# Kernel tuning notes

Measured on AMD Instinct MI355X. Metric: run time of the kernel, lower is better.

The kernel has to match this reference:

```python
import jax, jax.numpy as jnp
import numpy as np

D_MODEL = 1024
H = 16
D_K = D_MODEL // H
NEG = -1.0e9


def setup_inputs() -> dict:
    key = jax.random.key(0)
    ks = jax.random.split(key, 12)
    B, S = 2, 2048
    s = 1.0 / np.sqrt(D_MODEL)
    inp = {
        "q": jax.random.normal(ks[0], (B, S, D_MODEL), jnp.float32),
        "k": jax.random.normal(ks[1], (B, S, D_MODEL), jnp.float32),
        "v": jax.random.normal(ks[2], (B, S, D_MODEL), jnp.float32),
        "mask": jnp.tril(jnp.ones((S, S), jnp.int32))[None, None, :, :],
        "wq": jax.random.normal(ks[3], (D_MODEL, D_MODEL), jnp.float32) * s,
        "bq": jax.random.normal(ks[4], (D_MODEL,), jnp.float32) * s,
        "wk": jax.random.normal(ks[5], (D_MODEL, D_MODEL), jnp.float32) * s,
        "bk": jax.random.normal(ks[6], (D_MODEL,), jnp.float32) * s,
        "wv": jax.random.normal(ks[7], (D_MODEL, D_MODEL), jnp.float32) * s,
        "bv": jax.random.normal(ks[8], (D_MODEL,), jnp.float32) * s,
        "wo": jax.random.normal(ks[9], (D_MODEL, D_MODEL), jnp.float32) * s,
        "bo": jax.random.normal(ks[10], (D_MODEL,), jnp.float32) * s,
    }
    return inp


def _split_heads(x):
    # [B,S,D] -> [B,H,S,d_k]
    B, S, _ = x.shape
    return x.reshape(B, S, H, D_K).transpose(0, 2, 1, 3)


def reference(q, k, v, mask, wq, bq, wk, bk, wv, bv, wo, bo):
    # torch Linear: y = x @ W.T + b
    query = _split_heads(q @ wq.T + bq)
    key = _split_heads(k @ wk.T + bk)
    value = _split_heads(v @ wv.T + bv)
    # scores: [B,H,S,S]
    scores = jnp.einsum("bhqd,bhkd->bhqk", query, key) / jnp.sqrt(
        jnp.asarray(D_K, query.dtype))
    scores = jnp.where(mask == 0, jnp.asarray(NEG, scores.dtype), scores)
    attn = jax.nn.softmax(scores, axis=-1)  # dropout p=0.0 -> identity
    x = jnp.einsum("bhqk,bhkd->bhqd", attn, value)
    B, _, S, _ = x.shape
    x = x.transpose(0, 2, 1, 3).reshape(B, S, D_MODEL)
    return x @ wo.T + bo
```

## Files before the change

kernel.cpp:

```cpp
#include <hip/hip_runtime.h>
#include <hip/hip_bf16.h>
#include <cstdint>
#include <cstddef>

#define BATCH 2
#define SEQ   2048
#define DM    1024
#define NH    16
#define DK    64
#define MROWS (BATCH*SEQ)

typedef __bf16 bf16;
typedef float  f32x4  __attribute__((ext_vector_type(4)));
typedef bf16   bf16x8 __attribute__((ext_vector_type(8)));
typedef bf16   bf16x4 __attribute__((ext_vector_type(4)));

#define MFMA32(a, b, c) __builtin_amdgcn_mfma_f32_16x16x32_bf16(a, b, c, 0, 0, 0)

__device__ __forceinline__ void llds16(const void* gc, void* l) {
    void* g = (void*)gc;
    __builtin_amdgcn_global_load_lds(
        (__attribute__((address_space(1))) uint32_t*)g,
        (__attribute__((address_space(3))) uint32_t*)l,
        16, 0, 0);
}

__global__ __launch_bounds__(256) void k_convert(
    const float* __restrict__ q, const float* __restrict__ k, const float* __restrict__ v,
    const float* __restrict__ wq, const float* __restrict__ wk, const float* __restrict__ wv,
    const float* __restrict__ wo,
    bf16* __restrict__ qb, bf16* __restrict__ kb, bf16* __restrict__ vb,
    bf16* __restrict__ wqb, bf16* __restrict__ wkb, bf16* __restrict__ wvb,
    bf16* __restrict__ wob) {
    long t = (long)blockIdx.x * blockDim.x + threadIdx.x;
    const long NQ = (long)MROWS * DM / 4;
    const long NW = (long)DM * DM / 4;
    const float* src; bf16* dst; long off;
    if (t < NQ)            { src = q;  dst = qb;  off = t; }
    else if (t < 2*NQ)     { src = k;  dst = kb;  off = t - NQ; }
    else if (t < 3*NQ)     { src = v;  dst = vb;  off = t - 2*NQ; }
    else {
        long u = t - 3*NQ;
        if (u < NW)        { src = wq; dst = wqb; off = u; }
        else if (u < 2*NW) { src = wk; dst = wkb; off = u - NW; }
        else if (u < 3*NW) { src = wv; dst = wvb; off = u - 2*NW; }
        else               { src = wo; dst = wob; off = u - 3*NW; }
    }
    f32x4 x = *(const f32x4*)(src + off * 4);
    bf16x4 y;
    y[0] = (bf16)x[0]; y[1] = (bf16)x[1]; y[2] = (bf16)x[2]; y[3] = (bf16)x[3];
    *(bf16x4*)(dst + off * 4) = y;
}

__global__ __launch_bounds__(512, 8) void k_gemm_qkv(
    const bf16* __restrict__ qb, const bf16* __restrict__ kb, const bf16* __restrict__ vb,
    const bf16* __restrict__ wqb, const bf16* __restrict__ wkb, const bf16* __restrict__ wvb,
    const float* __restrict__ bq, const float* __restrict__ bk, const float* __restrict__ bv,
    bf16* __restrict__ Qf, bf16* __restrict__ Kf, bf16* __restrict__ Vf) {
    const int z = blockIdx.z;
    const int bid = blockIdx.x;
    const bf16* A; const bf16* B; const float* bias;
    int m0, n0;
    if (z == 2) {
        A = vb; B = wvb; bias = bv;
        m0 = (bid >> 4) * 128;
        n0 = (bid & 15) * 64;
    } else {
        A = z ? wkb : wqb; B = z ? kb : qb; bias = z ? bk : bq;
        m0 = (bid >> 6) * 128;
        n0 = (bid & 63) * 64;
    }

    constexpr int K = DM, BK = 64;
    __shared__ bf16 sA[128 * BK];
    __shared__ bf16 sB[64 * BK];
    const int tid = threadIdx.x;
    const int l = tid & 63, w = tid >> 6;
    const int quad = l >> 4, l15 = l & 15;
    const int wm = w & 1, wn = w >> 1;
    const int srow = l >> 3;
    const int scol = ((l & 7) ^ srow) * 8;

    f32x4 acc[4] = {};
    for (int k0 = 0; k0 < K; k0 += BK) {
#pragma unroll
        for (int i = 0; i < 2; ++i) {
            int g8 = (w * 2 + i) * 8;
            llds16(A + (size_t)(m0 + g8 + srow) * K + k0 + scol, &sA[g8 * BK]);
        }
        {
            int g8 = w * 8;
            llds16(B + (size_t)(n0 + g8 + srow) * K + k0 + scol, &sB[g8 * BK]);
        }
        __syncthreads();

#pragma unroll
        for (int kk = 0; kk < 2; ++kk) {
            bf16x8 af[4], bfr;
            {
                int row = wn * 16 + l15;
                int byt = (row * 128 + kk * 64 + quad * 16) ^ ((row & 7) << 4);
                bfr = *(const bf16x8*)((const char*)sB + byt);
            }
#pragma unroll
            for (int mi = 0; mi < 4; ++mi) {
                int row = wm * 64 + mi * 16 + l15;
                int byt = (row * 128 + kk * 64 + quad * 16) ^ ((row & 7) << 4);
                af[mi] = *(const bf16x8*)((const char*)sA + byt);
            }
#pragma unroll
            for (int mi = 0; mi < 4; ++mi)
                acc[mi] = MFMA32(af[mi], bfr, acc[mi]);
        }
        __syncthreads();
    }

    if (z == 2) {
        int dcol = n0 + wn * 16 + l15;
        int hh2 = dcol >> 6;
        int dtile = (dcol >> 4) & 3;
        float bias_v = bias[dcol];
#pragma unroll
        for (int mi = 0; mi < 4; ++mi) {
            int srw = m0 + wm * 64 + mi * 16;
            int bb = srw >> 11, sl = srw & 2047;
            int kc = sl >> 5;
            bf16x4 pack;
#pragma unroll
            for (int r = 0; r < 4; ++r)
                pack[r] = (bf16)(acc[mi][r] + bias_v);
            size_t entry = ((size_t)(bb * NH + hh2) * 64 + kc) * 4 + dtile;
            *(bf16x4*)(Vf + entry * 512 + (size_t)(quad * 16 + l15) * 8 + (mi & 1) * 4) = pack;
        }
    } else {
        bf16* out = z ? Kf : Qf;
        const float scale = z ? 1.0f : 0.18033688f;
        int scolg = n0 + wn * 16 + l15;
        int bb = scolg >> 11, s = scolg & 2047;
        int s16 = s >> 4;
#pragma unroll
        for (int mi = 0; mi < 4; ++mi) {
            int drow = m0 + wm * 64 + mi * 16;
            int hh2 = (drow >> 6) & 15;
            int chunk = (drow & 63) >> 5;
            int qp = 2 * (mi & 1) + (quad >> 1);
            bf16x4 pack;
#pragma unroll
            for (int r = 0; r < 4; ++r)
                pack[r] = (bf16)((acc[mi][r] + bias[drow + quad * 4 + r]) * scale);
            size_t entry = ((size_t)(bb * NH + hh2) * 128 + s16) * 2 + chunk;
            *(bf16x4*)(out + entry * 512 + (size_t)(qp * 16 + l15) * 8 + (quad & 1) * 4) = pack;
        }
    }
}

__global__ __launch_bounds__(512, 4) void k_gemm_out(
    const bf16* __restrict__ X, const bf16* __restrict__ wob,
    const float* __restrict__ bo, float* __restrict__ out) {
    constexpr int K = DM, BK = 64, NS = K / BK;
    const int m0 = blockIdx.y * 128, n0 = blockIdx.x * 64;
    __shared__ bf16 sA[2][128 * BK];
    __shared__ bf16 sB[2][64 * BK];
    const int tid = threadIdx.x;
    const int l = tid & 63, w = tid >> 6;
    const int quad = l >> 4, l15 = l & 15;
    const int wm = w & 1, wn = w >> 1;
    const int srow = l >> 3;
    const int scol = ((l & 7) ^ srow) * 8;

#pragma unroll
    for (int i = 0; i < 2; ++i) {
        int g8 = (w * 2 + i) * 8;
        llds16(X + (size_t)(m0 + g8 + srow) * K + scol, &sA[0][g8 * BK]);
    }
    llds16(wob + (size_t)(n0 + w * 8 + srow) * K + scol, &sB[0][(w * 8) * BK]);

    f32x4 acc[4] = {};
    for (int s = 0; s < NS; ++s) {
        __syncthreads();
        const int cur = s & 1;
        if (s + 1 < NS) {
            const int k0 = (s + 1) * BK;
#pragma unroll
            for (int i = 0; i < 2; ++i) {
                int g8 = (w * 2 + i) * 8;
                llds16(X + (size_t)(m0 + g8 + srow) * K + k0 + scol, &sA[cur ^ 1][g8 * BK]);
            }
            llds16(wob + (size_t)(n0 + w * 8 + srow) * K + k0 + scol, &sB[cur ^ 1][(w * 8) * BK]);
        }

#pragma unroll
        for (int kk = 0; kk < 2; ++kk) {
            bf16x8 af[4], bfr;
            {
                int row = wn * 16 + l15;
                int byt = (row * 128 + kk * 64 + quad * 16) ^ ((row & 7) << 4);
                bfr = *(const bf16x8*)((const char*)&sB[cur][0] + byt);
            }
#pragma unroll
            for (int mi = 0; mi < 4; ++mi) {
                int row = wm * 64 + mi * 16 + l15;
                int byt = (row * 128 + kk * 64 + quad * 16) ^ ((row & 7) << 4);
                af[mi] = *(const bf16x8*)((const char*)&sA[cur][0] + byt);
            }
#pragma unroll
            for (int mi = 0; mi < 4; ++mi)
                acc[mi] = MFMA32(af[mi], bfr, acc[mi]);
        }
    }
    {
        int col = n0 + wn * 16 + l15;
        float bias_v = bo[col];
#pragma unroll
        for (int mi = 0; mi < 4; ++mi) {
            int rbase = m0 + wm * 64 + mi * 16 + quad * 4;
#pragma unroll
            for (int r = 0; r < 4; ++r)
                out[(size_t)(rbase + r) * DM + col] = acc[mi][r] + bias_v;
        }
    }
}

__global__ __launch_bounds__(256, 4) void k_flash(const bf16* __restrict__ Qf,
                                                  const bf16* __restrict__ Kf,
                                                  const bf16* __restrict__ Vf,
                                                  bf16* __restrict__ X) {
    const int bh = blockIdx.x;
    const int qt = 31 - (int)blockIdx.y;
    const int b = bh >> 4, h = bh & 15;
    const int tid = threadIdx.x, w = tid >> 6, l = tid & 63;
    const int quad = l >> 4, l15 = l & 15;
    __shared__ bf16 sKV[2][16 * 512];

    const bf16* qfp = Qf + (size_t)bh * 128 * 1024;
    const bf16* kfp = Kf + (size_t)bh * 128 * 1024;
    const bf16* vfp = Vf + (size_t)bh * 64 * 4 * 512;

    const int qt16 = qt * 4 + w;
    const int qglob = qt16 * 16 + l15;

    bf16x8 qf[2];
#pragma unroll
    for (int c = 0; c < 2; ++c)
        qf[c] = *(const bf16x8*)(qfp + ((size_t)qt16 * 2 + c) * 512 + (size_t)l * 8);

    f32x4 o[4] = {};
    float lp = 0.f;

#pragma unroll
    for (int i = 0; i < 4; ++i) {
        int e = w * 4 + i;
        const bf16* src = (e < 8) ? kfp + ((size_t)e) * 512
                                  : vfp + ((size_t)(e - 8)) * 512;
        llds16(src + (size_t)l * 8, &sKV[0][e * 512]);
    }

    for (int j = 0; j <= qt; ++j) {
        __syncthreads();
        const bf16* cur = sKV[j & 1];
        if (j < qt) {
            int j1 = j + 1;
#pragma unroll
            for (int i = 0; i < 4; ++i) {
                int e = w * 4 + i;
                const bf16* src = (e < 8) ? kfp + ((size_t)(j1 * 8 + e)) * 512
                                          : vfp + ((size_t)(j1 * 8 + (e - 8))) * 512;
                llds16(src + (size_t)l * 8, (void*)&sKV[j1 & 1][e * 512]);
            }
        }

        f32x4 st[4];
#pragma unroll
        for (int ni = 0; ni < 4; ++ni) {
            bf16x8 k0 = *(const bf16x8*)&cur[(size_t)(ni * 2 + 0) * 512 + l * 8];
            bf16x8 k1 = *(const bf16x8*)&cur[(size_t)(ni * 2 + 1) * 512 + l * 8];
            f32x4 zz = {};
            zz = MFMA32(k0, qf[0], zz);
            st[ni] = MFMA32(k1, qf[1], zz);
        }

        const bool diag = (j == qt);
#pragma unroll
        for (int c = 0; c < 2; ++c) {
            bf16x8 pb;
#pragma unroll
            for (int half = 0; half < 2; ++half) {
                int ni = 2 * c + half;
#pragma unroll
                for (int r = 0; r < 4; ++r) {
                    float s = st[ni][r];
                    if (diag) {
                        int key = j * 64 + ni * 16 + quad * 4 + r;
                        if (key > qglob) s = -1e30f;
                    }
                    float e = __builtin_amdgcn_exp2f(s);
                    lp += e;
                    pb[half * 4 + r] = (bf16)e;
                }
            }
#pragma unroll
            for (int dt = 0; dt < 4; ++dt) {
                bf16x8 vv = *(const bf16x8*)&cur[(size_t)(8 + c * 4 + dt) * 512 + l * 8];
                o[dt] = MFMA32(vv, pb, o[dt]);
            }
        }
    }

    lp += __shfl_xor(lp, 16, 64);
    lp += __shfl_xor(lp, 32, 64);
    float rv = 1.f / lp;

    __syncthreads();
    bf16* Xw = &sKV[0][w * 16 * 72];
#pragma unroll
    for (int dt = 0; dt < 4; ++dt) {
        bf16x4 pk;
#pragma unroll
        for (int r = 0; r < 4; ++r)
            pk[r] = (bf16)(o[dt][r] * rv);
        *(bf16x4*)&Xw[l15 * 72 + dt * 16 + quad * 4] = pk;
    }
#pragma unroll
    for (int i = 0; i < 2; ++i) {
        int row = i * 8 + (l >> 3);
        bf16x8 vv = *(const bf16x8*)&Xw[row * 72 + (l & 7) * 8];
        *(bf16x8*)(X + (size_t)(b * SEQ + qt16 * 16 + row) * DM + h * 64 + (l & 7) * 8) = vv;
    }
}

extern "C" void kernel_launch(void* const* d_in, const int* in_sizes, int n_in,
                              void* d_out, int out_size, void* d_ws, size_t ws_size,
                              hipStream_t stream) {
    const float* q  = (const float*)d_in[0];
    const float* k  = (const float*)d_in[1];
    const float* v  = (const float*)d_in[2];
    const float* wq = (const float*)d_in[4];
    const float* bq = (const float*)d_in[5];
    const float* wk = (const float*)d_in[6];
    const float* bk = (const float*)d_in[7];
    const float* wv = (const float*)d_in[8];
    const float* bv = (const float*)d_in[9];
    const float* wo = (const float*)d_in[10];
    const float* bo = (const float*)d_in[11];
    float* out = (float*)d_out;

    uint8_t* ws = (uint8_t*)d_ws;
    const size_t SZ_ACT = (size_t)MROWS * DM * sizeof(bf16);
    const size_t SZ_W   = (size_t)DM * DM * sizeof(bf16);
    bf16* qb  = (bf16*)(ws);
    bf16* kb  = (bf16*)(ws + SZ_ACT);
    bf16* vb  = (bf16*)(ws + 2 * SZ_ACT);
    bf16* wqb = (bf16*)(ws + 3 * SZ_ACT);
    bf16* wkb = (bf16*)(ws + 3 * SZ_ACT + SZ_W);
    bf16* wvb = (bf16*)(ws + 3 * SZ_ACT + 2 * SZ_W);
    bf16* wob = (bf16*)(ws + 3 * SZ_ACT + 3 * SZ_W);
    bf16* Qf  = (bf16*)(ws + 3 * SZ_ACT + 4 * SZ_W);
    bf16* Kf  = (bf16*)(ws + 4 * SZ_ACT + 4 * SZ_W);
    bf16* Vf  = (bf16*)(ws + 5 * SZ_ACT + 4 * SZ_W);
    bf16* X   = (bf16*)(ws + 6 * SZ_ACT + 4 * SZ_W);

    {
        long total_vec4 = 3L * MROWS * DM / 4 + 4L * DM * DM / 4;
        k_convert<<<dim3((unsigned)(total_vec4 / 256)), 256, 0, stream>>>(
            q, k, v, wq, wk, wv, wo, qb, kb, vb, wqb, wkb, wvb, wob);
    }
    k_gemm_qkv<<<dim3(512, 1, 3), 512, 0, stream>>>(
        qb, kb, vb, wqb, wkb, wvb, bq, bk, bv, Qf, Kf, Vf);
    k_flash<<<dim3(BATCH * NH, SEQ / 64), 256, 0, stream>>>(Qf, Kf, Vf, X);
    k_gemm_out<<<dim3(DM / 64, MROWS / 128), 512, 0, stream>>>(X, wob, bo, out);
}
```

Baseline: 207.0 us.

## Enlarge QKV GEMM block tile to 128x128 with 4 waves of 64x64

The QKV projection GEMM moves from a 128x64 tile run by 8 waves to a 128x128 tile run by 4 waves, each computing a 64x64 sub-tile of 16 MFMA accumulators. The grid and block size are adjusted to match. This raises per-wave register reuse of A and B fragments and cuts LDS and global traffic per MFMA. In exchange it uses more accumulator registers, allows lower occupancy, and launches fewer, larger blocks.

```diff
diff --git a/kernel.cpp b/kernel.cpp
--- a/kernel.cpp
+++ b/kernel.cpp
@@ -52,7 +52,7 @@
     *(bf16x4*)(dst + off * 4) = y;
 }
 
-__global__ __launch_bounds__(512, 8) void k_gemm_qkv(
+__global__ __launch_bounds__(256, 4) void k_gemm_qkv(
     const bf16* __restrict__ qb, const bf16* __restrict__ kb, const bf16* __restrict__ vb,
     const bf16* __restrict__ wqb, const bf16* __restrict__ wkb, const bf16* __restrict__ wvb,
     const float* __restrict__ bq, const float* __restrict__ bk, const float* __restrict__ bv,
@@ -63,17 +63,17 @@
     int m0, n0;
     if (z == 2) {
         A = vb; B = wvb; bias = bv;
-        m0 = (bid >> 4) * 128;
-        n0 = (bid & 15) * 64;
+        m0 = (bid >> 3) * 128;
+        n0 = (bid & 7) * 128;
     } else {
         A = z ? wkb : wqb; B = z ? kb : qb; bias = z ? bk : bq;
-        m0 = (bid >> 6) * 128;
-        n0 = (bid & 63) * 64;
+        m0 = (bid >> 5) * 128;
+        n0 = (bid & 31) * 128;
     }
 
     constexpr int K = DM, BK = 64;
     __shared__ bf16 sA[128 * BK];
-    __shared__ bf16 sB[64 * BK];
+    __shared__ bf16 sB[128 * BK];
     const int tid = threadIdx.x;
     const int l = tid & 63, w = tid >> 6;
     const int quad = l >> 4, l15 = l & 15;
@@ -81,27 +81,19 @@
     const int srow = l >> 3;
     const int scol = ((l & 7) ^ srow) * 8;
 
-    f32x4 acc[4] = {};
+    f32x4 acc[4][4] = {};
     for (int k0 = 0; k0 < K; k0 += BK) {
 #pragma unroll
-        for (int i = 0; i < 2; ++i) {
-            int g8 = (w * 2 + i) * 8;
-            llds16(A + (size_t)(m0 + g8 + srow) * K + k0 + scol, &sA[g8 * BK]);
-        }
-        {
-            int g8 = w * 8;
-            llds16(B + (size_t)(n0 + g8 + srow) * K + k0 + scol, &sB[g8 * BK]);
+        for (int i = 0; i < 4; ++i) {
+            int r8 = (w * 4 + i) * 8;
+            llds16(A + (size_t)(m0 + r8 + srow) * K + k0 + scol, &sA[r8 * BK]);
+            llds16(B + (size_t)(n0 + r8 + srow) * K + k0 + scol, &sB[r8 * BK]);
         }
         __syncthreads();
 
 #pragma unroll
         for (int kk = 0; kk < 2; ++kk) {
-            bf16x8 af[4], bfr;
-            {
-                int row = wn * 16 + l15;
-                int byt = (row * 128 + kk * 64 + quad * 16) ^ ((row & 7) << 4);
-                bfr = *(const bf16x8*)((const char*)sB + byt);
-            }
+            bf16x8 af[4], bfr[4];
 #pragma unroll
             for (int mi = 0; mi < 4; ++mi) {
                 int row = wm * 64 + mi * 16 + l15;
@@ -109,47 +101,67 @@
                 af[mi] = *(const bf16x8*)((const char*)sA + byt);
             }
 #pragma unroll
+            for (int ni = 0; ni < 4; ++ni) {
+                int row = wn * 64 + ni * 16 + l15;
+                int byt = (row * 128 + kk * 64 + quad * 16) ^ ((row & 7) << 4);
+                bfr[ni] = *(const bf16x8*)((const char*)sB + byt);
+            }
+#pragma unroll
             for (int mi = 0; mi < 4; ++mi)
-                acc[mi] = MFMA32(af[mi], bfr, acc[mi]);
+#pragma unroll
+                for (int ni = 0; ni < 4; ++ni)
+                    acc[mi][ni] = MFMA32(af[mi], bfr[ni], acc[mi][ni]);
         }
         __syncthreads();
     }
 
     if (z == 2) {
-        int dcol = n0 + wn * 16 + l15;
-        int hh2 = dcol >> 6;
-        int dtile = (dcol >> 4) & 3;
-        float bias_v = bias[dcol];
-#pragma unroll
-        for (int mi = 0; mi < 4; ++mi) {
-            int srw = m0 + wm * 64 + mi * 16;
-            int bb = srw >> 11, sl = srw & 2047;
-            int kc = sl >> 5;
-            bf16x4 pack;
-#pragma unroll
-            for (int r = 0; r < 4; ++r)
-                pack[r] = (bf16)(acc[mi][r] + bias_v);
-            size_t entry = ((size_t)(bb * NH + hh2) * 64 + kc) * 4 + dtile;
-            *(bf16x4*)(Vf + entry * 512 + (size_t)(quad * 16 + l15) * 8 + (mi & 1) * 4) = pack;
+#pragma unroll
+        for (int ni = 0; ni < 4; ++ni) {
+            int dcol = n0 + wn * 64 + ni * 16 + l15;
+            int hh2 = dcol >> 6;
+            int dtile = (dcol >> 4) & 3;
+            float bias_v = bias[dcol];
+#pragma unroll
+            for (int mi = 0; mi < 4; ++mi) {
+                int srw = m0 + wm * 64 + mi * 16;
+                int bb = srw >> 11, sl = srw & 2047;
+                int kc = sl >> 5;
+                bf16x4 pack;
+#pragma unroll
+                for (int r = 0; r < 4; ++r)
+                    pack[r] = (bf16)(acc[mi][ni][r] + bias_v);
+                size_t entry = ((size_t)(bb * NH + hh2) * 64 + kc) * 4 + dtile;
+                *(bf16x4*)(Vf + entry * 512 + (size_t)(quad * 16 + l15) * 8 + (mi & 1) * 4) = pack;
+            }
         }
     } else {
         bf16* out = z ? Kf : Qf;
         const float scale = z ? 1.0f : 0.18033688f;
-        int scolg = n0 + wn * 16 + l15;
-        int bb = scolg >> 11, s = scolg & 2047;
-        int s16 = s >> 4;
-#pragma unroll
-        for (int mi = 0; mi < 4; ++mi) {
-            int drow = m0 + wm * 64 + mi * 16;
-            int hh2 = (drow >> 6) & 15;
-            int chunk = (drow & 63) >> 5;
-            int qp = 2 * (mi & 1) + (quad >> 1);
-            bf16x4 pack;
+        float bias_rv[4][4];
+#pragma unroll
+        for (int mi = 0; mi < 4; ++mi)
 #pragma unroll
             for (int r = 0; r < 4; ++r)
-                pack[r] = (bf16)((acc[mi][r] + bias[drow + quad * 4 + r]) * scale);
-            size_t entry = ((size_t)(bb * NH + hh2) * 128 + s16) * 2 + chunk;
-            *(bf16x4*)(out + entry * 512 + (size_t)(qp * 16 + l15) * 8 + (quad & 1) * 4) = pack;
+                bias_rv[mi][r] = bias[m0 + wm * 64 + mi * 16 + quad * 4 + r];
+#pragma unroll
+        for (int ni = 0; ni < 4; ++ni) {
+            int scolg = n0 + wn * 64 + ni * 16 + l15;
+            int bb = scolg >> 11, s = scolg & 2047;
+            int s16 = s >> 4;
+#pragma unroll
+            for (int mi = 0; mi < 4; ++mi) {
+                int drow = m0 + wm * 64 + mi * 16;
+                int hh2 = (drow >> 6) & 15;
+                int chunk = (drow & 63) >> 5;
+                int qp = 2 * (mi & 1) + (quad >> 1);
+                bf16x4 pack;
+#pragma unroll
+                for (int r = 0; r < 4; ++r)
+                    pack[r] = (bf16)((acc[mi][ni][r] + bias_rv[mi][r]) * scale);
+                size_t entry = ((size_t)(bb * NH + hh2) * 128 + s16) * 2 + chunk;
+                *(bf16x4*)(out + entry * 512 + (size_t)(qp * 16 + l15) * 8 + (quad & 1) * 4) = pack;
+            }
         }
     }
 }
@@ -364,7 +376,7 @@
         k_convert<<<dim3((unsigned)(total_vec4 / 256)), 256, 0, stream>>>(
             q, k, v, wq, wk, wv, wo, qb, kb, vb, wqb, wkb, wvb, wob);
     }
-    k_gemm_qkv<<<dim3(512, 1, 3), 512, 0, stream>>>(
+    k_gemm_qkv<<<dim3(256, 1, 3), 256, 0, stream>>>(
         qb, kb, vb, wqb, wkb, wvb, bq, bk, bv, Qf, Kf, Vf);
     k_flash<<<dim3(BATCH * NH, SEQ / 64), 256, 0, stream>>>(Qf, Kf, Vf, X);
     k_gemm_out<<<dim3(DM / 64, MROWS / 128), 512, 0, stream>>>(X, wob, bo, out);
```

Measured after the change: 210.1 us. No clear change (+1.5%).
